# Optimization experiments

Hardware: AMD Instinct MI355X
Metric: run time of the kernel (lower is better)

## Reference

```python
import jax, jax.numpy as jnp
import numpy as np

N = 50000   # nodes
E = 800000  # edges per order
F = 128     # input features (== hidden so layers stack)
H = 128     # hidden
C = 10      # classes
L = 3       # num_layers
O = 2       # Order (max_petal_dim)
K = 10      # propagation hops
G = 128     # num graphs in batch
ALPHA = 0.5
EPS = 1e-5  # BatchNorm eps


def _fw_init():
    # HiGCN_prop.reset_parameters: fW[k] = alpha*(1-alpha)^k, fW[K] = (1-alpha)^K
    fw = np.array([ALPHA * (1 - ALPHA) ** k for k in range(K + 1)], dtype=np.float32)
    fw[-1] = (1 - ALPHA) ** K
    return jnp.broadcast_to(jnp.asarray(fw), (L, O, K + 1))


def setup_inputs() -> dict:
    key = jax.random.key(0)
    ks = iter(jax.random.split(key, 64))
    nk = lambda: next(ks)
    s = lambda shape: (jax.random.normal(nk(), shape, jnp.float32) * 0.05)
    x = jax.random.normal(nk(), (N, F), jnp.float32)
    edge_index = jax.random.randint(nk(), (O, 2, E), 0, N, dtype=jnp.int32)
    # scale weights so expected row sum ~0.5 -> stable over K=10 hops
    edge_weight = jax.random.uniform(nk(), (O, E), jnp.float32) * (1.0 / 16.0)
    batch = jnp.sort(jax.random.randint(nk(), (N,), 0, G, dtype=jnp.int32))
    return {
        "x": x, "edge_index": edge_index, "edge_weight": edge_weight, "batch": batch,
        "W_in": s((L, O, F, H)), "b_in": s((L, O, H)),
        "fW": _fw_init(),
        "W_out": s((L, O * H, H)), "b_out": s((L, H)),
        "Wn1": s((L, H, H)), "bn1": s((L, H)), "g1": jnp.ones((L, H), jnp.float32), "be1": s((L, H)),
        "Wn2": s((L, H, H)), "bn2": s((L, H)), "g2": jnp.ones((L, H), jnp.float32), "be2": s((L, H)),
        "W1": s((H, H)), "b1": s((H,)), "W2": s((H, C)), "b2": s((C,)),
    }


def _bn(x, g, b):
    # eval-mode BatchNorm1d: running_mean=0, running_var=1
    return x * (g / jnp.sqrt(1.0 + EPS)) + b


def _spmm(dst, src, w, h):
    # out[dst] += w * h[src]  == matmul(HL, h, reduce='add')
    return jax.ops.segment_sum(w[:, None] * h[src], dst, num_segments=N)


def reference(x, edge_index, edge_weight, batch, W_in, b_in, fW, W_out, b_out,
              Wn1, bn1, g1, be1, Wn2, bn2, g2, be2, W1, b1, W2, b2):
    h = x
    for l in range(L):
        outs = []
        for o in range(O):
            dst, src = edge_index[o, 0], edge_index[o, 1]
            w = edge_weight[o]
            z = h @ W_in[l, o] + b_in[l, o]           # [N, H]
            hid = fW[l, o, 0] * z
            for k in range(K):
                z = _spmm(dst, src, w, z)
                hid = hid + fW[l, o, k + 1] * z
            outs.append(hid)
        xc = jnp.concatenate(outs, axis=1) @ W_out[l] + b_out[l]   # [N, H]
        xc = jnp.maximum(_bn(xc @ Wn1[l] + bn1[l], g1[l], be1[l]), 0.0)
        h = jnp.maximum(_bn(xc @ Wn2[l] + bn2[l], g2[l], be2[l]), 0.0)
    p = jax.ops.segment_sum(h, batch, num_segments=G)              # global_add_pool [G, H]
    p = jnp.maximum(p @ W1 + b1, 0.0)
    return p @ W2 + b2                                             # [G, C]
```

## Files before the change

### kernel.cpp

```cpp
#include <hip/hip_runtime.h>

#define NNODES 50000
#define NEDGES 800000
#define HDIM 128
#define CDIM 10
#define LNUM 3
#define ONUM 2
#define KHOPS 10
#define GNUM 128
#define EPSBN 1e-5f

typedef unsigned int uint;
typedef unsigned short ushort;
typedef __attribute__((ext_vector_type(8))) short bf16x8;
typedef __attribute__((ext_vector_type(4))) float f32x4;

__device__ __forceinline__ ushort f2bf(float f) {
    uint u = __builtin_bit_cast(uint, f);
    uint r = (u + 0x7fffu + ((u >> 16) & 1u)) >> 16;
    return (ushort)r;
}
__device__ __forceinline__ float bf2f_lo(uint u) { return __builtin_bit_cast(float, u << 16); }
__device__ __forceinline__ float bf2f_hi(uint u) { return __builtin_bit_cast(float, u & 0xffff0000u); }

#define KC 128
#define LDA 136
__global__ __launch_bounds__(256) void mfma_gemm(
    const float* __restrict__ A0, const float* __restrict__ A1,
    const ushort* __restrict__ Wt, int Kdim,
    const float* __restrict__ bias, const float* __restrict__ g,
    const float* __restrict__ be, const float* __restrict__ fw0,
    float* __restrict__ outf, ushort* __restrict__ outz,
    float* __restrict__ hid, int relu)
{
    __shared__ ushort sA[64 * LDA];
    __shared__ ushort sB[128 * LDA];
    const int row0 = blockIdx.x * 64;
    const int tid  = threadIdx.x;
    const int w    = tid >> 6;
    const int lane = tid & 63;
    const int lr   = lane & 15;
    const int q    = lane >> 4;

    f32x4 acc[8];
#pragma unroll
    for (int nt = 0; nt < 8; ++nt)
#pragma unroll
        for (int j = 0; j < 4; ++j) acc[nt][j] = 0.f;

    const int nch = A1 ? 2 : 1;
    for (int c = 0; c < nch; ++c) {
        const float* Asrc = c ? A1 : A0;
        for (int idx = tid; idx < 64 * 64; idx += 256) {
            int r = idx >> 6, kp = idx & 63;
            int row = row0 + r;
            float2 v = make_float2(0.f, 0.f);
            if (row < NNODES) v = ((const float2*)(Asrc + (size_t)row * HDIM))[kp];
            uint pv = (uint)f2bf(v.x) | ((uint)f2bf(v.y) << 16);
            ((uint*)(sA + r * LDA))[kp] = pv;
        }
        for (int idx = tid; idx < 128 * 64; idx += 256) {
            int n = idx >> 6, kp = idx & 63;
            uint u = ((const uint*)(Wt + (size_t)n * Kdim + c * KC))[kp];
            ((uint*)(sB + n * LDA))[kp] = u;
        }
        __syncthreads();
#pragma unroll
        for (int kt = 0; kt < 4; ++kt) {
            bf16x8 a = *(const bf16x8*)(sA + (16 * w + lr) * LDA + kt * 32 + q * 8);
#pragma unroll
            for (int nt = 0; nt < 8; ++nt) {
                bf16x8 b = *(const bf16x8*)(sB + (nt * 16 + lr) * LDA + kt * 32 + q * 8);
                acc[nt] = __builtin_amdgcn_mfma_f32_16x16x32_bf16(a, b, acc[nt], 0, 0, 0);
            }
        }
        __syncthreads();
    }

    const float f0 = fw0 ? fw0[0] : 0.f;
#pragma unroll
    for (int nt = 0; nt < 8; ++nt) {
        int col = nt * 16 + lr;
        float bs = bias[col];
        float sc = 1.f, bt = 0.f;
        if (g) { sc = g[col] * rsqrtf(1.f + EPSBN); bt = be[col]; }
#pragma unroll
        for (int r = 0; r < 4; ++r) {
            int row = row0 + 16 * w + q * 4 + r;
            if (row >= NNODES) continue;
            float v = acc[nt][r] + bs;
            if (g) v = v * sc + bt;
            if (relu) v = fmaxf(v, 0.f);
            size_t off = (size_t)row * HDIM + col;
            if (outf) outf[off] = v;
            if (outz) outz[off] = f2bf(v);
            if (hid)  hid[off]  = f0 * v;
        }
    }
}

__global__ void wtrans_all(const float* __restrict__ W_in, const float* __restrict__ W_out,
                           const float* __restrict__ Wn1, const float* __restrict__ Wn2,
                           ushort* __restrict__ Wt_in, ushort* __restrict__ Wt_out,
                           ushort* __restrict__ Wt_n1, ushort* __restrict__ Wt_n2)
{
    int b = blockIdx.x;
    const float* W; ushort* Wt; int Kd;
    if (b < 6)       { Kd = HDIM;     W = W_in  + (size_t)b * Kd * HDIM;       Wt = Wt_in  + (size_t)b * Kd * HDIM; }
    else if (b < 9)  { Kd = 2 * HDIM; W = W_out + (size_t)(b - 6) * Kd * HDIM; Wt = Wt_out + (size_t)(b - 6) * Kd * HDIM; }
    else if (b < 12) { Kd = HDIM;     W = Wn1   + (size_t)(b - 9) * Kd * HDIM; Wt = Wt_n1  + (size_t)(b - 9) * Kd * HDIM; }
    else             { Kd = HDIM;     W = Wn2   + (size_t)(b - 12) * Kd * HDIM; Wt = Wt_n2 + (size_t)(b - 12) * Kd * HDIM; }
    for (int idx = threadIdx.x; idx < Kd * HDIM; idx += 512) {
        int k = idx >> 7, n = idx & 127;
        Wt[(size_t)n * Kd + k] = f2bf(W[idx]);
    }
}

__global__ void gemm_rows(const float* __restrict__ A0,
                          const float* __restrict__ W, const float* __restrict__ bias,
                          float* __restrict__ out, int N, int Hout, int relu)
{
    __shared__ float a[8][HDIM];
    const int row0 = blockIdx.x * 8;
    const int tid  = threadIdx.x;
    for (int r = 0; r < 8; ++r) {
        int row = row0 + r;
        a[r][tid] = (row < N) ? A0[(size_t)row * HDIM + tid] : 0.f;
    }
    __syncthreads();
    if (tid < Hout) {
        float acc[8];
#pragma unroll
        for (int r = 0; r < 8; ++r) acc[r] = 0.f;
        for (int k = 0; k < HDIM; ++k) {
            float wv = W[(size_t)k * Hout + tid];
#pragma unroll
            for (int r = 0; r < 8; ++r) acc[r] += a[r][k] * wv;
        }
        const float bs = bias[tid];
        for (int r = 0; r < 8; ++r) {
            int row = row0 + r;
            if (row >= N) break;
            float v = acc[r] + bs;
            if (relu) v = fmaxf(v, 0.f);
            out[(size_t)row * Hout + tid] = v;
        }
    }
}

__global__ void hist2(const int* __restrict__ ei, int* __restrict__ cur0, int* __restrict__ cur1)
{
    int e = blockIdx.x * blockDim.x + threadIdx.x;
    if (e >= NEDGES) return;
    int o = blockIdx.y;
    const int* dst = ei + (size_t)o * 2 * NEDGES;
    atomicAdd((o ? cur1 : cur0) + dst[e], 1);
}

__global__ __launch_bounds__(1024) void scan2(int* __restrict__ cur0, int* __restrict__ rp0,
                                              int* __restrict__ cur1, int* __restrict__ rp1)
{
    int* cursor = blockIdx.x ? cur1 : cur0;
    int* rowptr = blockIdx.x ? rp1 : rp0;
    __shared__ int wsum[16];
    __shared__ int carry;
    const int lane = threadIdx.x & 63, w = threadIdx.x >> 6;
    if (threadIdx.x == 0) carry = 0;
    __syncthreads();
    for (int base = 0; base < NNODES; base += 4096) {
        int i4 = base + threadIdx.x * 4;
        int4 v = make_int4(0, 0, 0, 0);
        if (i4 + 3 < NNODES) v = *(const int4*)(cursor + i4);
        int s0 = v.x, s1 = s0 + v.y, s2 = s1 + v.z, s3 = s2 + v.w;
        int q = s3;
#pragma unroll
        for (int d = 1; d < 64; d <<= 1) {
            int u = __shfl_up(q, d, 64);
            if (lane >= d) q += u;
        }
        if (lane == 63) wsum[w] = q;
        __syncthreads();
        if (w == 0) {
            int s = (lane < 16) ? wsum[lane] : 0;
#pragma unroll
            for (int d = 1; d < 16; d <<= 1) {
                int u = __shfl_up(s, d, 64);
                if (lane >= d) s += u;
            }
            if (lane < 16) wsum[lane] = s;
        }
        __syncthreads();
        int excl = carry + ((w > 0) ? wsum[w - 1] : 0) + (q - s3);
        if (i4 + 3 < NNODES) {
            int4 o4 = make_int4(excl, excl + s0, excl + s1, excl + s2);
            *(int4*)(rowptr + i4) = o4;
            *(int4*)(cursor + i4) = o4;
        }
        __syncthreads();
        if (threadIdx.x == 1023) carry += wsum[15];
        __syncthreads();
    }
    if (threadIdx.x == 0) rowptr[NNODES] = carry;
}

__global__ void fill2(const int* __restrict__ ei, const float* __restrict__ ew,
                      int* __restrict__ cur0, int* __restrict__ cur1,
                      int2* __restrict__ c0, int2* __restrict__ c1)
{
    int e = blockIdx.x * blockDim.x + threadIdx.x;
    if (e >= NEDGES) return;
    int o = blockIdx.y;
    const int* dst = ei + (size_t)o * 2 * NEDGES;
    const int* src = dst + NEDGES;
    const float* wp = ew + (size_t)o * NEDGES;
    int pos = atomicAdd((o ? cur1 : cur0) + dst[e], 1);
    (o ? c1 : c0)[pos] = make_int2(src[e], __builtin_bit_cast(int, wp[e]));
}

__global__ void spmm2(const int* __restrict__ rp0, const int2* __restrict__ csr0,
                      const int* __restrict__ rp1, const int2* __restrict__ csr1,
                      const ushort* __restrict__ zin0, ushort* __restrict__ zout0,
                      const ushort* __restrict__ zin1, ushort* __restrict__ zout1,
                      float* __restrict__ hid0, float* __restrict__ hid1,
                      const float* __restrict__ fw0p, const float* __restrict__ fw1p,
                      int do_hid)
{
    int node = blockIdx.x * 4 + (threadIdx.x >> 6);
    if (node >= NNODES) return;
    const int o = blockIdx.y;
    const int lane = threadIdx.x & 63;
    const int*  rp  = o ? rp1 : rp0;
    const int2* csr = o ? csr1 : csr0;
    const ushort* zin = o ? zin1 : zin0;
    ushort* zout = o ? zout1 : zout0;
    float* hid = o ? hid1 : hid0;
    const float* fwp = o ? fw1p : fw0p;

    int beg = __builtin_amdgcn_readfirstlane(rp[node]);
    int end = __builtin_amdgcn_readfirstlane(rp[node + 1]);
    float ax = 0.f, ay = 0.f;
    int j = beg;
    for (; j + 3 < end; j += 4) {
        int2 e0 = csr[j], e1 = csr[j + 1], e2 = csr[j + 2], e3 = csr[j + 3];
        uint u0 = ((const uint*)(zin + (size_t)e0.x * HDIM))[lane];
        uint u1 = ((const uint*)(zin + (size_t)e1.x * HDIM))[lane];
        uint u2 = ((const uint*)(zin + (size_t)e2.x * HDIM))[lane];
        uint u3 = ((const uint*)(zin + (size_t)e3.x * HDIM))[lane];
        float w0 = __builtin_bit_cast(float, e0.y), w1 = __builtin_bit_cast(float, e1.y);
        float w2 = __builtin_bit_cast(float, e2.y), w3 = __builtin_bit_cast(float, e3.y);
        ax += w0 * bf2f_lo(u0) + w1 * bf2f_lo(u1) + w2 * bf2f_lo(u2) + w3 * bf2f_lo(u3);
        ay += w0 * bf2f_hi(u0) + w1 * bf2f_hi(u1) + w2 * bf2f_hi(u2) + w3 * bf2f_hi(u3);
    }
    for (; j < end; ++j) {
        int2 e = csr[j];
        uint u = ((const uint*)(zin + (size_t)e.x * HDIM))[lane];
        float wt = __builtin_bit_cast(float, e.y);
        ax += wt * bf2f_lo(u);
        ay += wt * bf2f_hi(u);
    }
    ((uint*)(zout + (size_t)node * HDIM))[lane] = (uint)f2bf(ax) | ((uint)f2bf(ay) << 16);
    if (do_hid) {
        uint up = ((const uint*)(zin + (size_t)node * HDIM))[lane];
        const float c0 = fwp[0], c1 = fwp[1];
        float2* hp = (float2*)(hid + (size_t)node * HDIM);
        float2 h = hp[lane];
        h.x += c0 * bf2f_lo(up) + c1 * ax;
        h.y += c0 * bf2f_hi(up) + c1 * ay;
        hp[lane] = h;
    }
}

__global__ __launch_bounds__(1024) void pool_seg(const float* __restrict__ h,
                                                 const int* __restrict__ batch,
                                                 float* __restrict__ pool)
{
    __shared__ float red[1024];
    const int gph = blockIdx.x;
    const int t  = threadIdx.x & 127;
    const int rr = threadIdx.x >> 7;
    int lo = 0, hi = NNODES;
    while (lo < hi) { int m = (lo + hi) >> 1; if (batch[m] < gph) lo = m + 1; else hi = m; }
    const int beg = lo;
    hi = NNODES;
    while (lo < hi) { int m = (lo + hi) >> 1; if (batch[m] < gph + 1) lo = m + 1; else hi = m; }
    const int end = lo;
    float acc = 0.f;
    for (int i = beg + rr; i < end; i += 8) acc += h[(size_t)i * HDIM + t];
    red[threadIdx.x] = acc;
    __syncthreads();
    if (rr == 0) {
        float s = 0.f;
#pragma unroll
        for (int k = 0; k < 8; ++k) s += red[t + 128 * k];
        pool[(size_t)gph * HDIM + t] = s;
    }
}

extern "C" void kernel_launch(void* const* d_in, const int* in_sizes, int n_in,
                              void* d_out, int out_size, void* d_ws, size_t ws_size,
                              hipStream_t stream)
{
    const float* x     = (const float*)d_in[0];
    const int*   ei    = (const int*)  d_in[1];
    const float* ew    = (const float*)d_in[2];
    const int*   batch = (const int*)  d_in[3];
    const float* W_in  = (const float*)d_in[4];
    const float* b_in  = (const float*)d_in[5];
    const float* fW    = (const float*)d_in[6];
    const float* W_out = (const float*)d_in[7];
    const float* b_out = (const float*)d_in[8];
    const float* Wn1   = (const float*)d_in[9];
    const float* bn1   = (const float*)d_in[10];
    const float* g1    = (const float*)d_in[11];
    const float* be1   = (const float*)d_in[12];
    const float* Wn2   = (const float*)d_in[13];
    const float* bn2   = (const float*)d_in[14];
    const float* g2    = (const float*)d_in[15];
    const float* be2   = (const float*)d_in[16];
    const float* W1    = (const float*)d_in[17];
    const float* b1    = (const float*)d_in[18];
    const float* W2    = (const float*)d_in[19];
    const float* b2    = (const float*)d_in[20];
    float* out = (float*)d_out;

    const size_t NH = (size_t)NNODES * HDIM;
    float* ws  = (float*)d_ws;
    float*  f_A = ws;
    float*  f_B = ws + NH;
    ushort* z0A = (ushort*)(ws + 2 * NH);
    ushort* z0B = z0A + NH;
    ushort* z1A = z0B + NH;
    ushort* z1B = z1A + NH;
    float*  f_pl  = (float*)(z1B + NH);
    float*  f_pl2 = f_pl + (size_t)GNUM * HDIM;

    ushort* Wt_in  = (ushort*)(f_pl2 + (size_t)GNUM * HDIM);
    ushort* Wt_out = Wt_in  + (size_t)6 * HDIM * HDIM;
    ushort* Wt_n1  = Wt_out + (size_t)3 * 2 * HDIM * HDIM;
    ushort* Wt_n2  = Wt_n1  + (size_t)3 * HDIM * HDIM;

    int*  rowptr0 = (int*)(Wt_n2 + (size_t)3 * HDIM * HDIM);
    int*  rowptr1 = rowptr0 + (NNODES + 1);
    int*  cursor0 = rowptr1 + (NNODES + 1);
    int*  cursor1 = cursor0 + NNODES;
    int2* csr0    = (int2*)(cursor1 + NNODES);
    int2* csr1    = csr0 + NEDGES;

    const int gemm_grid = (NNODES + 63) / 64;
    const int edge_grid = (NEDGES + 255) / 256;
    const dim3 spmm_grid((NNODES + 3) / 4, 2);

    wtrans_all<<<15, 512, 0, stream>>>(W_in, W_out, Wn1, Wn2, Wt_in, Wt_out, Wt_n1, Wt_n2);

    hipMemsetAsync(cursor0, 0, 2 * NNODES * sizeof(int), stream);
    hist2<<<dim3(edge_grid, 2), 256, 0, stream>>>(ei, cursor0, cursor1);
    scan2<<<2, 1024, 0, stream>>>(cursor0, rowptr0, cursor1, rowptr1);
    fill2<<<dim3(edge_grid, 2), 256, 0, stream>>>(ei, ew, cursor0, cursor1, csr0, csr1);

    const float* curH = x;
    for (int l = 0; l < LNUM; ++l) {
        float* h0 = (curH == (const float*)f_A) ? f_B : f_A;
        float* h1 = (l == 0) ? f_B : (float*)curH;
        const int lo0 = l * ONUM, lo1 = lo0 + 1;
        mfma_gemm<<<gemm_grid, 256, 0, stream>>>(
            curH, nullptr, Wt_in + (size_t)lo0 * HDIM * HDIM, HDIM,
            b_in + (size_t)lo0 * HDIM, nullptr, nullptr,
            fW + (size_t)lo0 * (KHOPS + 1), nullptr, z0A, h0, 0);
        mfma_gemm<<<gemm_grid, 256, 0, stream>>>(
            curH, nullptr, Wt_in + (size_t)lo1 * HDIM * HDIM, HDIM,
            b_in + (size_t)lo1 * HDIM, nullptr, nullptr,
            fW + (size_t)lo1 * (KHOPS + 1), nullptr, z1A, h1, 0);

        ushort *pa0 = z0A, *pb0 = z0B, *pa1 = z1A, *pb1 = z1B;
        for (int k = 1; k <= KHOPS; ++k) {
            spmm2<<<spmm_grid, 256, 0, stream>>>(
                rowptr0, csr0, rowptr1, csr1, pa0, pb0, pa1, pb1, h0, h1,
                fW + (size_t)lo0 * (KHOPS + 1) + (k - 1),
                fW + (size_t)lo1 * (KHOPS + 1) + (k - 1),
                (k & 1) == 0);
            ushort* t;
            t = pa0; pa0 = pb0; pb0 = t;
            t = pa1; pa1 = pb1; pb1 = t;
        }
        mfma_gemm<<<gemm_grid, 256, 0, stream>>>(
            h0, h1, Wt_out + (size_t)l * 2 * HDIM * HDIM, 2 * HDIM,
            b_out + (size_t)l * HDIM, nullptr, nullptr, nullptr,
            h0, nullptr, nullptr, 0);
        mfma_gemm<<<gemm_grid, 256, 0, stream>>>(
            h0, nullptr, Wt_n1 + (size_t)l * HDIM * HDIM, HDIM,
            bn1 + (size_t)l * HDIM, g1 + (size_t)l * HDIM, be1 + (size_t)l * HDIM,
            nullptr, h1, nullptr, nullptr, 1);
        mfma_gemm<<<gemm_grid, 256, 0, stream>>>(
            h1, nullptr, Wt_n2 + (size_t)l * HDIM * HDIM, HDIM,
            bn2 + (size_t)l * HDIM, g2 + (size_t)l * HDIM, be2 + (size_t)l * HDIM,
            nullptr, h0, nullptr, nullptr, 1);
        curH = h0;
    }

    pool_seg<<<GNUM, 1024, 0, stream>>>(curH, batch, f_pl);
    gemm_rows<<<(GNUM + 7) / 8, 128, 0, stream>>>(f_pl,  W1, b1, f_pl2, GNUM, HDIM, 1);
    gemm_rows<<<(GNUM + 7) / 8, 128, 0, stream>>>(f_pl2, W2, b2, out,   GNUM, CDIM, 0);
}
```

Baseline: 2.808 ms.

## Replace CSR with fixed-width packed ELL buckets and split features into planes

```diff
diff --git a/kernel.cpp b/kernel.cpp
--- a/kernel.cpp
+++ b/kernel.cpp
@@ -9,6 +9,7 @@
 #define KHOPS 10
 #define GNUM 128
 #define EPSBN 1e-5f
+#define ZPL ((size_t)NNODES * 64)
 
 typedef unsigned int uint;
 typedef unsigned short ushort;
@@ -31,8 +32,12 @@
     const float* __restrict__ bias, const float* __restrict__ g,
     const float* __restrict__ be, const float* __restrict__ fw0,
     float* __restrict__ outf, ushort* __restrict__ outz,
-    float* __restrict__ hid, int relu)
-{
+    float* __restrict__ hid, int relu,
+    const ushort* __restrict__ Wt_b, const float* __restrict__ bias_b,
+    const float* __restrict__ fw0_b, ushort* __restrict__ outz_b,
+    float* __restrict__ hid_b)
+{
+    if (blockIdx.y) { Wt = Wt_b; bias = bias_b; fw0 = fw0_b; outz = outz_b; hid = hid_b; }
     __shared__ ushort sA[64 * LDA];
     __shared__ ushort sB[128 * LDA];
     const int row0 = blockIdx.x * 64;
@@ -91,10 +96,9 @@
             float v = acc[nt][r] + bs;
             if (g) v = v * sc + bt;
             if (relu) v = fmaxf(v, 0.f);
-            size_t off = (size_t)row * HDIM + col;
-            if (outf) outf[off] = v;
-            if (outz) outz[off] = f2bf(v);
-            if (hid)  hid[off]  = f0 * v;
+            if (outf) outf[(size_t)row * HDIM + col] = v;
+            if (outz) outz[(size_t)(col >> 6) * ZPL + (size_t)row * 64 + (col & 63)] = f2bf(v);
+            if (hid)  hid[(size_t)row * HDIM + col] = f0 * v;
         }
     }
 }
@@ -106,10 +110,10 @@
 {
     int b = blockIdx.x;
     const float* W; ushort* Wt; int Kd;
-    if (b < 6)       { Kd = HDIM;     W = W_in  + (size_t)b * Kd * HDIM;       Wt = Wt_in  + (size_t)b * Kd * HDIM; }
-    else if (b < 9)  { Kd = 2 * HDIM; W = W_out + (size_t)(b - 6) * Kd * HDIM; Wt = Wt_out + (size_t)(b - 6) * Kd * HDIM; }
-    else if (b < 12) { Kd = HDIM;     W = Wn1   + (size_t)(b - 9) * Kd * HDIM; Wt = Wt_n1  + (size_t)(b - 9) * Kd * HDIM; }
-    else             { Kd = HDIM;     W = Wn2   + (size_t)(b - 12) * Kd * HDIM; Wt = Wt_n2 + (size_t)(b - 12) * Kd * HDIM; }
+    if (b < 6)       { Kd = HDIM;     W = W_in  + (size_t)b * Kd * HDIM;        Wt = Wt_in  + (size_t)b * Kd * HDIM; }
+    else if (b < 9)  { Kd = 2 * HDIM; W = W_out + (size_t)(b - 6) * Kd * HDIM;  Wt = Wt_out + (size_t)(b - 6) * Kd * HDIM; }
+    else if (b < 12) { Kd = HDIM;     W = Wn1   + (size_t)(b - 9) * Kd * HDIM;  Wt = Wt_n1  + (size_t)(b - 9) * Kd * HDIM; }
+    else             { Kd = HDIM;     W = Wn2   + (size_t)(b - 12) * Kd * HDIM; Wt = Wt_n2  + (size_t)(b - 12) * Kd * HDIM; }
     for (int idx = threadIdx.x; idx < Kd * HDIM; idx += 512) {
         int k = idx >> 7, n = idx & 127;
         Wt[(size_t)n * Kd + k] = f2bf(W[idx]);
@@ -148,125 +152,75 @@
     }
 }
 
-__global__ void hist2(const int* __restrict__ ei, int* __restrict__ cur0, int* __restrict__ cur1)
-{
-    int e = blockIdx.x * blockDim.x + threadIdx.x;
-    if (e >= NEDGES) return;
-    int o = blockIdx.y;
-    const int* dst = ei + (size_t)o * 2 * NEDGES;
-    atomicAdd((o ? cur1 : cur0) + dst[e], 1);
-}
-
-__global__ __launch_bounds__(1024) void scan2(int* __restrict__ cur0, int* __restrict__ rp0,
-                                              int* __restrict__ cur1, int* __restrict__ rp1)
-{
-    int* cursor = blockIdx.x ? cur1 : cur0;
-    int* rowptr = blockIdx.x ? rp1 : rp0;
-    __shared__ int wsum[16];
-    __shared__ int carry;
-    const int lane = threadIdx.x & 63, w = threadIdx.x >> 6;
-    if (threadIdx.x == 0) carry = 0;
-    __syncthreads();
-    for (int base = 0; base < NNODES; base += 4096) {
-        int i4 = base + threadIdx.x * 4;
-        int4 v = make_int4(0, 0, 0, 0);
-        if (i4 + 3 < NNODES) v = *(const int4*)(cursor + i4);
-        int s0 = v.x, s1 = s0 + v.y, s2 = s1 + v.z, s3 = s2 + v.w;
-        int q = s3;
-#pragma unroll
-        for (int d = 1; d < 64; d <<= 1) {
-            int u = __shfl_up(q, d, 64);
-            if (lane >= d) q += u;
-        }
-        if (lane == 63) wsum[w] = q;
-        __syncthreads();
-        if (w == 0) {
-            int s = (lane < 16) ? wsum[lane] : 0;
-#pragma unroll
-            for (int d = 1; d < 16; d <<= 1) {
-                int u = __shfl_up(s, d, 64);
-                if (lane >= d) s += u;
-            }
-            if (lane < 16) wsum[lane] = s;
-        }
-        __syncthreads();
-        int excl = carry + ((w > 0) ? wsum[w - 1] : 0) + (q - s3);
-        if (i4 + 3 < NNODES) {
-            int4 o4 = make_int4(excl, excl + s0, excl + s1, excl + s2);
-            *(int4*)(rowptr + i4) = o4;
-            *(int4*)(cursor + i4) = o4;
-        }
-        __syncthreads();
-        if (threadIdx.x == 1023) carry += wsum[15];
-        __syncthreads();
-    }
-    if (threadIdx.x == 0) rowptr[NNODES] = carry;
-}
-
 __global__ void fill2(const int* __restrict__ ei, const float* __restrict__ ew,
-                      int* __restrict__ cur0, int* __restrict__ cur1,
-                      int2* __restrict__ c0, int2* __restrict__ c1)
+                      int* __restrict__ cnt0, int* __restrict__ cnt1,
+                      uint* __restrict__ bk0, uint* __restrict__ bk1)
 {
     int e = blockIdx.x * blockDim.x + threadIdx.x;
     if (e >= NEDGES) return;
     int o = blockIdx.y;
     const int* dst = ei + (size_t)o * 2 * NEDGES;
     const int* src = dst + NEDGES;
-    const float* wp = ew + (size_t)o * NEDGES;
-    int pos = atomicAdd((o ? cur1 : cur0) + dst[e], 1);
-    (o ? c1 : c0)[pos] = make_int2(src[e], __builtin_bit_cast(int, wp[e]));
-}
-
-__global__ void spmm2(const int* __restrict__ rp0, const int2* __restrict__ csr0,
-                      const int* __restrict__ rp1, const int2* __restrict__ csr1,
+    float w = ew[(size_t)o * NEDGES + e];
+    int d = dst[e];
+    int pos = atomicAdd((o ? cnt1 : cnt0) + d, 1);
+    if (pos < 64)
+        (o ? bk1 : bk0)[((size_t)d << 6) + pos] = ((uint)f2bf(w) << 16) | (uint)src[e];
+}
+
+__global__ void spmm2(const int* __restrict__ cnt0, const uint* __restrict__ bk0,
+                      const int* __restrict__ cnt1, const uint* __restrict__ bk1,
                       const ushort* __restrict__ zin0, ushort* __restrict__ zout0,
                       const ushort* __restrict__ zin1, ushort* __restrict__ zout1,
                       float* __restrict__ hid0, float* __restrict__ hid1,
                       const float* __restrict__ fw0p, const float* __restrict__ fw1p,
                       int do_hid)
 {
-    int node = blockIdx.x * 4 + (threadIdx.x >> 6);
+    const int o     = blockIdx.y & 1;
+    const int plane = blockIdx.y >> 1;
+    const int lane  = threadIdx.x & 63;
+    const int half  = lane >> 5;
+    const int l31   = lane & 31;
+    const int node  = blockIdx.x * 8 + ((threadIdx.x >> 6) << 1) + half;
     if (node >= NNODES) return;
-    const int o = blockIdx.y;
-    const int lane = threadIdx.x & 63;
-    const int*  rp  = o ? rp1 : rp0;
-    const int2* csr = o ? csr1 : csr0;
-    const ushort* zin = o ? zin1 : zin0;
-    ushort* zout = o ? zout1 : zout0;
-    float* hid = o ? hid1 : hid0;
+
+    const int*  cnt = o ? cnt1 : cnt0;
+    const uint* bk  = o ? bk1 : bk0;
+    const uint* zi  = (const uint*)((o ? zin1 : zin0) + plane * ZPL);
+    uint*       zo  = (uint*)((o ? zout1 : zout0) + plane * ZPL);
+    float*      hid = o ? hid1 : hid0;
     const float* fwp = o ? fw1p : fw0p;
 
-    int beg = __builtin_amdgcn_readfirstlane(rp[node]);
-    int end = __builtin_amdgcn_readfirstlane(rp[node + 1]);
+    int n = cnt[node]; n = n > 64 ? 64 : n;
+    const uint* b = bk + ((size_t)node << 6);
     float ax = 0.f, ay = 0.f;
-    int j = beg;
-    for (; j + 3 < end; j += 4) {
-        int2 e0 = csr[j], e1 = csr[j + 1], e2 = csr[j + 2], e3 = csr[j + 3];
-        uint u0 = ((const uint*)(zin + (size_t)e0.x * HDIM))[lane];
-        uint u1 = ((const uint*)(zin + (size_t)e1.x * HDIM))[lane];
-        uint u2 = ((const uint*)(zin + (size_t)e2.x * HDIM))[lane];
-        uint u3 = ((const uint*)(zin + (size_t)e3.x * HDIM))[lane];
-        float w0 = __builtin_bit_cast(float, e0.y), w1 = __builtin_bit_cast(float, e1.y);
-        float w2 = __builtin_bit_cast(float, e2.y), w3 = __builtin_bit_cast(float, e3.y);
+    int j = 0;
+    for (; j + 3 < n; j += 4) {
+        uint e0 = b[j], e1 = b[j + 1], e2 = b[j + 2], e3 = b[j + 3];
+        uint u0 = zi[(size_t)(e0 & 0xffffu) * 32 + l31];
+        uint u1 = zi[(size_t)(e1 & 0xffffu) * 32 + l31];
+        uint u2 = zi[(size_t)(e2 & 0xffffu) * 32 + l31];
+        uint u3 = zi[(size_t)(e3 & 0xffffu) * 32 + l31];
+        float w0 = bf2f_hi(e0), w1 = bf2f_hi(e1), w2 = bf2f_hi(e2), w3 = bf2f_hi(e3);
         ax += w0 * bf2f_lo(u0) + w1 * bf2f_lo(u1) + w2 * bf2f_lo(u2) + w3 * bf2f_lo(u3);
         ay += w0 * bf2f_hi(u0) + w1 * bf2f_hi(u1) + w2 * bf2f_hi(u2) + w3 * bf2f_hi(u3);
     }
-    for (; j < end; ++j) {
-        int2 e = csr[j];
-        uint u = ((const uint*)(zin + (size_t)e.x * HDIM))[lane];
-        float wt = __builtin_bit_cast(float, e.y);
+    for (; j < n; ++j) {
+        uint e = b[j];
+        uint u = zi[(size_t)(e & 0xffffu) * 32 + l31];
+        float wt = bf2f_hi(e);
         ax += wt * bf2f_lo(u);
         ay += wt * bf2f_hi(u);
     }
-    ((uint*)(zout + (size_t)node * HDIM))[lane] = (uint)f2bf(ax) | ((uint)f2bf(ay) << 16);
+    zo[(size_t)node * 32 + l31] = (uint)f2bf(ax) | ((uint)f2bf(ay) << 16);
     if (do_hid) {
-        uint up = ((const uint*)(zin + (size_t)node * HDIM))[lane];
+        uint up = zi[(size_t)node * 32 + l31];
         const float c0 = fwp[0], c1 = fwp[1];
-        float2* hp = (float2*)(hid + (size_t)node * HDIM);
-        float2 h = hp[lane];
+        float2* hp = (float2*)hid + (size_t)node * 64 + plane * 32 + l31;
+        float2 h = *hp;
         h.x += c0 * bf2f_lo(up) + c1 * ax;
         h.y += c0 * bf2f_hi(up) + c1 * ay;
-        hp[lane] = h;
+        *hp = h;
     }
 }
 
@@ -339,42 +293,35 @@
     ushort* Wt_n1  = Wt_out + (size_t)3 * 2 * HDIM * HDIM;
     ushort* Wt_n2  = Wt_n1  + (size_t)3 * HDIM * HDIM;
 
-    int*  rowptr0 = (int*)(Wt_n2 + (size_t)3 * HDIM * HDIM);
-    int*  rowptr1 = rowptr0 + (NNODES + 1);
-    int*  cursor0 = rowptr1 + (NNODES + 1);
-    int*  cursor1 = cursor0 + NNODES;
-    int2* csr0    = (int2*)(cursor1 + NNODES);
-    int2* csr1    = csr0 + NEDGES;
+    int*  cnt0 = (int*)(Wt_n2 + (size_t)3 * HDIM * HDIM);
+    int*  cnt1 = cnt0 + NNODES;
+    uint* bk0  = (uint*)(cnt1 + NNODES);
+    uint* bk1  = bk0 + ((size_t)NNODES << 6);
 
     const int gemm_grid = (NNODES + 63) / 64;
     const int edge_grid = (NEDGES + 255) / 256;
-    const dim3 spmm_grid((NNODES + 3) / 4, 2);
+    const dim3 spmm_grid((NNODES + 7) / 8, 4);
 
     wtrans_all<<<15, 512, 0, stream>>>(W_in, W_out, Wn1, Wn2, Wt_in, Wt_out, Wt_n1, Wt_n2);
-
-    hipMemsetAsync(cursor0, 0, 2 * NNODES * sizeof(int), stream);
-    hist2<<<dim3(edge_grid, 2), 256, 0, stream>>>(ei, cursor0, cursor1);
-    scan2<<<2, 1024, 0, stream>>>(cursor0, rowptr0, cursor1, rowptr1);
-    fill2<<<dim3(edge_grid, 2), 256, 0, stream>>>(ei, ew, cursor0, cursor1, csr0, csr1);
+    hipMemsetAsync(cnt0, 0, 2 * NNODES * sizeof(int), stream);
+    fill2<<<dim3(edge_grid, 2), 256, 0, stream>>>(ei, ew, cnt0, cnt1, bk0, bk1);
 
     const float* curH = x;
     for (int l = 0; l < LNUM; ++l) {
         float* h0 = (curH == (const float*)f_A) ? f_B : f_A;
         float* h1 = (l == 0) ? f_B : (float*)curH;
         const int lo0 = l * ONUM, lo1 = lo0 + 1;
-        mfma_gemm<<<gemm_grid, 256, 0, stream>>>(
+        mfma_gemm<<<dim3(gemm_grid, 2), 256, 0, stream>>>(
             curH, nullptr, Wt_in + (size_t)lo0 * HDIM * HDIM, HDIM,
             b_in + (size_t)lo0 * HDIM, nullptr, nullptr,
-            fW + (size_t)lo0 * (KHOPS + 1), nullptr, z0A, h0, 0);
-        mfma_gemm<<<gemm_grid, 256, 0, stream>>>(
-            curH, nullptr, Wt_in + (size_t)lo1 * HDIM * HDIM, HDIM,
-            b_in + (size_t)lo1 * HDIM, nullptr, nullptr,
-            fW + (size_t)lo1 * (KHOPS + 1), nullptr, z1A, h1, 0);
+            fW + (size_t)lo0 * (KHOPS + 1), nullptr, z0A, h0, 0,
+            Wt_in + (size_t)lo1 * HDIM * HDIM, b_in + (size_t)lo1 * HDIM,
+            fW + (size_t)lo1 * (KHOPS + 1), z1A, h1);
 
         ushort *pa0 = z0A, *pb0 = z0B, *pa1 = z1A, *pb1 = z1B;
         for (int k = 1; k <= KHOPS; ++k) {
             spmm2<<<spmm_grid, 256, 0, stream>>>(
-                rowptr0, csr0, rowptr1, csr1, pa0, pb0, pa1, pb1, h0, h1,
+                cnt0, bk0, cnt1, bk1, pa0, pb0, pa1, pb1, h0, h1,
                 fW + (size_t)lo0 * (KHOPS + 1) + (k - 1),
                 fW + (size_t)lo1 * (KHOPS + 1) + (k - 1),
                 (k & 1) == 0);
@@ -385,15 +332,18 @@
         mfma_gemm<<<gemm_grid, 256, 0, stream>>>(
             h0, h1, Wt_out + (size_t)l * 2 * HDIM * HDIM, 2 * HDIM,
             b_out + (size_t)l * HDIM, nullptr, nullptr, nullptr,
-            h0, nullptr, nullptr, 0);
+            h0, nullptr, nullptr, 0,
+            nullptr, nullptr, nullptr, nullptr, nullptr);
         mfma_gemm<<<gemm_grid, 256, 0, stream>>>(
             h0, nullptr, Wt_n1 + (size_t)l * HDIM * HDIM, HDIM,
             bn1 + (size_t)l * HDIM, g1 + (size_t)l * HDIM, be1 + (size_t)l * HDIM,
-            nullptr, h1, nullptr, nullptr, 1);
+            nullptr, h1, nullptr, nullptr, 1,
+            nullptr, nullptr, nullptr, nullptr, nullptr);
         mfma_gemm<<<gemm_grid, 256, 0, stream>>>(
             h1, nullptr, Wt_n2 + (size_t)l * HDIM * HDIM, HDIM,
             bn2 + (size_t)l * HDIM, g2 + (size_t)l * HDIM, be2 + (size_t)l * HDIM,
-            nullptr, h0, nullptr, nullptr, 1);
+            nullptr, h0, nullptr, nullptr, 1,
+            nullptr, nullptr, nullptr, nullptr, nullptr);
         curH = h0;
     }
 
```

Result: slower. 3.078 ms (+9.6%).
